# Kernel tuning notes

Hardware: AMD Instinct MI355X
Metric: run time of the kernel (lower is better)

The kernel has to match this reference:

```python
import jax, jax.numpy as jnp
import numpy as np

D_MODEL = 1024
N_HEADS = 16
DH = D_MODEL // N_HEADS
T = 64
NUM_REL = 15 * 15  # (2*7+1)^2 for 8x8 grid
B = 1024


def _build_rel_index(H=8, W=8, dx_max=7, dy_max=7):
    ys, xs = np.meshgrid(np.arange(H), np.arange(W), indexing='ij')
    coords = np.stack([xs.reshape(-1), ys.reshape(-1)], axis=-1)  # [T,2] (x,y)
    disp = coords[None, :, :] - coords[:, None, :]
    dx = np.clip(disp[..., 0], -dx_max, dx_max) + dx_max
    dy = np.clip(disp[..., 1], -dy_max, dy_max) + dy_max
    return jnp.asarray(dx + (2 * dx_max + 1) * dy, dtype=jnp.int32)  # [T,T]


def setup_inputs() -> dict:
    key = jax.random.key(0)
    ks = jax.random.split(key, 12)
    s = 0.02
    return {
        'x': jax.random.normal(ks[0], (B, T, D_MODEL), dtype=jnp.float32),
        'Wq_w': jax.random.normal(ks[1], (D_MODEL, D_MODEL), dtype=jnp.float32) * s,
        'Wq_b': jnp.zeros((D_MODEL,), dtype=jnp.float32),
        'Wk_w': jax.random.normal(ks[2], (D_MODEL, D_MODEL), dtype=jnp.float32) * s,
        'Wk_b': jnp.zeros((D_MODEL,), dtype=jnp.float32),
        'Wv_w': jax.random.normal(ks[3], (D_MODEL, D_MODEL), dtype=jnp.float32) * s,
        'Wv_b': jnp.zeros((D_MODEL,), dtype=jnp.float32),
        'Wo_w': jax.random.normal(ks[4], (D_MODEL, D_MODEL), dtype=jnp.float32) * s,
        'Wo_b': jnp.zeros((D_MODEL,), dtype=jnp.float32),
        'rel_q': jax.random.normal(ks[5], (N_HEADS, NUM_REL, DH), dtype=jnp.float32) * s,
        'rel_k': jax.random.normal(ks[6], (N_HEADS, NUM_REL, DH), dtype=jnp.float32) * s,
        'rel_v': jax.random.normal(ks[7], (N_HEADS, NUM_REL, DH), dtype=jnp.float32) * s,
        'rel_index': _build_rel_index(),
    }


def reference(x, Wq_w, Wq_b, Wk_w, Wk_b, Wv_w, Wv_b, Wo_w, Wo_b,
              rel_q, rel_k, rel_v, rel_index):
    Bb, Tt, D = x.shape
    H, dh = N_HEADS, DH
    scale = 1.0 / jnp.sqrt(jnp.asarray(dh, dtype=x.dtype))
    # projections (torch Linear: x @ W.T + b), split into heads -> [B,H,T,dh]
    q = (x @ Wq_w.T + Wq_b).reshape(Bb, Tt, H, dh).transpose(0, 2, 1, 3)
    k = (x @ Wk_w.T + Wk_b).reshape(Bb, Tt, H, dh).transpose(0, 2, 1, 3)
    v = (x @ Wv_w.T + Wv_b).reshape(Bb, Tt, H, dh).transpose(0, 2, 1, 3)
    # gather relative embeddings -> [H,T,T,dh]
    rq = rel_q[:, rel_index]
    rk = rel_k[:, rel_index]
    rv = rel_v[:, rel_index]
    qk = jnp.einsum('bhtd,bhsd->bhts', q, k)
    q_relk = jnp.einsum('bhtd,htsd->bhts', q, rk)
    relq_k = jnp.einsum('htsd,bhsd->bhts', rq, k)
    relq_relk = jnp.einsum('htsd,htsd->hts', rq, rk)
    logits = (qk + q_relk + relq_k + relq_relk[None]) * scale
    attn = jax.nn.softmax(logits, axis=-1)  # [B,H,T,T]
    out = jnp.einsum('bhts,bhsd->bhtd', attn, v) + jnp.einsum('bhts,htsd->bhtd', attn, rv)
    out = out.transpose(0, 2, 1, 3).reshape(Bb, Tt, D)
    return out @ Wo_w.T + Wo_b
```

## Files before the change

kernel.cpp:

```cpp
#include <hip/hip_runtime.h>

typedef __attribute__((ext_vector_type(4))) float f32x4;
typedef __attribute__((ext_vector_type(8))) short s16x8;
typedef __attribute__((ext_vector_type(4))) short s16x4;

__device__ __forceinline__ short f2bf(float f) {
  union { float f; unsigned u; } v; v.f = f;
  unsigned r = (v.u + 0x7fffu + ((v.u >> 16) & 1u)) >> 16;
  return (short)(r & 0xffffu);
}
__device__ __forceinline__ float bf2f(short s) {
  union { unsigned u; float f; } v; v.u = ((unsigned)(unsigned short)s) << 16;
  return v.f;
}
__device__ __forceinline__ f32x4 mfma16(s16x8 a, s16x8 b, f32x4 c) {
  return __builtin_amdgcn_mfma_f32_16x16x32_bf16(a, b, c, 0, 0, 0);
}

#define AS1(p) ((__attribute__((address_space(1))) void*)(p))
#define AS3(p) ((__attribute__((address_space(3))) void*)(p))

__global__ __launch_bounds__(256) void cvt_bf16_kernel(const float* __restrict__ in,
                                                       short* __restrict__ out, long n) {
  long i = ((long)blockIdx.x * 256 + threadIdx.x) * 4;
  if (i + 4 <= n) {
    f32x4 v = *(const f32x4*)(in + i);
    s16x4 o;
    o[0] = f2bf(v[0]); o[1] = f2bf(v[1]); o[2] = f2bf(v[2]); o[3] = f2bf(v[3]);
    *(s16x4*)(out + i) = o;
  }
}

__global__ __launch_bounds__(256) void bias_cat_kernel(const float* __restrict__ bq,
                                                       const float* __restrict__ bk,
                                                       const float* __restrict__ bv,
                                                       float* __restrict__ o) {
  int i = blockIdx.x * 256 + threadIdx.x;
  if (i < 3072) o[i] = (i < 1024) ? bq[i] : ((i < 2048) ? bk[i - 1024] : bv[i - 2048]);
}

__global__ __launch_bounds__(64) void prep_rel_kernel(
    const float* __restrict__ rq, const float* __restrict__ rk, const float* __restrict__ rv,
    short* __restrict__ relqb, short* __restrict__ relkb, short* __restrict__ relvT,
    float* __restrict__ Dh) {
  int h = blockIdx.x / 240;
  int r = blockIdx.x % 240;
  int d = threadIdx.x;
  float vq = 0.f, vk = 0.f, vv = 0.f;
  if (r < 225) {
    long o = ((long)h * 225 + r) * 64 + d;
    vq = rq[o]; vk = rk[o]; vv = rv[o];
  }
  relqb[((long)h * 240 + r) * 64 + d] = f2bf(vq);
  relkb[((long)h * 240 + r) * 64 + d] = f2bf(vk);
  relvT[((long)h * 64 + d) * 256 + r] = f2bf(vv);
  if (r < 16) relvT[((long)h * 64 + d) * 256 + 240 + r] = 0;
  float p = vq * vk;
  #pragma unroll
  for (int m = 32; m >= 1; m >>= 1) p += __shfl_xor(p, m);
  if (d == 0) Dh[h * 240 + r] = p;
}

#define BAR  __builtin_amdgcn_s_barrier()
#define LGK0 do { asm volatile("s_waitcnt lgkmcnt(0)" ::: "memory"); \
                  __builtin_amdgcn_sched_barrier(0); } while (0)
#define VM0  asm volatile("s_waitcnt vmcnt(0)" ::: "memory")
#define PRIO1 __builtin_amdgcn_s_setprio(1)
#define PRIO0 __builtin_amdgcn_s_setprio(0)

#define STG_A(D, H, KOFF) do { \
    const short* _s = gA + (long)(H) * 128 * ldaL + (KOFF); \
    char* _d = lds + (D) * 32768 + (H) * 16384 + ldsw; \
    __builtin_amdgcn_global_load_lds(AS1(_s), AS3(_d), 16, 0, 0); \
    __builtin_amdgcn_global_load_lds(AS1(_s + 64 * ldaL), AS3(_d + 8192), 16, 0, 0); \
  } while (0)
#define STG_B(D, H, KOFF) do { \
    const short* _s = gB + (long)(H) * 128 * ldbL + (KOFF); \
    char* _d = lds + 65536 + (D) * 32768 + (H) * 16384 + ldsw; \
    __builtin_amdgcn_global_load_lds(AS1(_s), AS3(_d), 16, 0, 0); \
    __builtin_amdgcn_global_load_lds(AS1(_s + 64 * ldbL), AS3(_d + 8192), 16, 0, 0); \
  } while (0)
#define RD_A(D, MIH) do { \
    const char* _b = lds + (D) * 32768 + baseA + (MIH) * 8192; \
    _Pragma("unroll") for (int i = 0; i < 4; i++) { \
      aa[0][i] = *(const s16x8*)(_b + i * 2048 + cax0); \
      aa[1][i] = *(const s16x8*)(_b + i * 2048 + cax1); \
    } } while (0)
#define RD_B(D, NJH) do { \
    const char* _b = lds + (D) * 32768 + baseB + (NJH) * 4096; \
    _Pragma("unroll") for (int j = 0; j < 2; j++) { \
      bb[0][(NJH) * 2 + j] = *(const s16x8*)(_b + j * 2048 + cax0); \
      bb[1][(NJH) * 2 + j] = *(const s16x8*)(_b + j * 2048 + cax1); \
    } } while (0)
#define MM_Q(MIH, NJH) do { \
    _Pragma("unroll") for (int i = 0; i < 4; i++) { \
      _Pragma("unroll") for (int j = 0; j < 2; j++) { \
        f32x4& c = acc[(MIH) * 4 + i][(NJH) * 2 + j]; \
        c = mfma16(bb[0][(NJH) * 2 + j], aa[0][i], c); \
        c = mfma16(bb[1][(NJH) * 2 + j], aa[1][i], c); \
    } } } while (0)

template<int OUT_BF16>
__global__ __launch_bounds__(512, 2) void gemm256_kernel(
    const short* __restrict__ A, const short* __restrict__ Bw,
    const float* __restrict__ bias, void* __restrict__ Cout,
    int N, int K, int lda) {
  __shared__ __attribute__((aligned(16))) char lds[131072];
  const int tid = threadIdx.x, lane = tid & 63, w = tid >> 6;
  const int wr = w >> 2, wc = w & 3;
  const int l15 = lane & 15, l4 = lane >> 4;
  const int nbn = N >> 8;
  const int nwg = gridDim.x, bid = blockIdx.x;
  const int swz = ((bid & 7) * (nwg >> 3)) + (bid >> 3);
  const int bm = swz / nbn, bn = swz % nbn;

  const int srow = tid >> 3;
  const int scol = ((tid & 7) ^ (srow & 7)) * 8;
  const long ldaL = lda, ldbL = K;
  const short* gA = A  + ((long)(bm * 256 + srow)) * ldaL + scol;
  const short* gB = Bw + ((long)(bn * 256 + srow)) * ldbL + scol;
  const int ldsw = w * 1024;

  const int baseA = (wr * 128 + l15) * 128;
  const int baseB = 65536 + (wc * 64 + l15) * 128;
  const int cax0 = ((l4) ^ (l15 & 7)) * 16;
  const int cax1 = ((4 + l4) ^ (l15 & 7)) * 16;

  f32x4 acc[8][4];
  #pragma unroll
  for (int i = 0; i < 8; i++)
    #pragma unroll
    for (int j = 0; j < 4; j++) acc[i][j] = (f32x4){0.f, 0.f, 0.f, 0.f};
  s16x8 aa[2][4], bb[2][4];

  STG_A(0, 0, 0); STG_A(0, 1, 0); STG_B(0, 0, 0); STG_B(0, 1, 0);
  STG_B(1, 0, 64); STG_B(1, 1, 64);
  VM0;
  BAR;

  const int NT = K >> 6;
  for (int kt = 0; kt < NT; kt += 2) {
    const int k1 = (kt + 1) << 6, k2 = (kt + 2) << 6, k3 = (kt + 3) << 6;
    const bool full = (kt + 2) < NT;
    STG_A(1, 0, k1);
    RD_A(0, 0); RD_B(0, 0);
    BAR; LGK0; PRIO1; MM_Q(0, 0); PRIO0; BAR;
    STG_A(1, 1, k1);
    RD_B(0, 1);
    BAR; LGK0; PRIO1; MM_Q(0, 1); PRIO0; BAR;
    if (full) STG_B(0, 0, k2);
    RD_A(0, 1);
    BAR; LGK0; PRIO1; MM_Q(1, 0); PRIO0; BAR;
    if (full) STG_B(0, 1, k2);
    BAR; LGK0; PRIO1; MM_Q(1, 1); PRIO0;
    VM0;
    BAR;
    if (full) STG_A(0, 0, k2);
    RD_A(1, 0); RD_B(1, 0);
    BAR; LGK0; PRIO1; MM_Q(0, 0); PRIO0; BAR;
    if (full) STG_A(0, 1, k2);
    RD_B(1, 1);
    BAR; LGK0; PRIO1; MM_Q(0, 1); PRIO0; BAR;
    if (full) STG_B(1, 0, k3);
    RD_A(1, 1);
    BAR; LGK0; PRIO1; MM_Q(1, 0); PRIO0; BAR;
    if (full) STG_B(1, 1, k3);
    BAR; LGK0; PRIO1; MM_Q(1, 1); PRIO0;
    VM0;
    BAR;
  }

  const long crow = (long)bm * 256 + wr * 128;
  const int ccol = bn * 256 + wc * 64;
  #pragma unroll
  for (int nj = 0; nj < 4; nj++) {
    const int colb = ccol + nj * 16 + l4 * 4;
    const f32x4 bv4 = *(const f32x4*)&bias[colb];
    #pragma unroll
    for (int mi = 0; mi < 8; mi++) {
      const long row = crow + mi * 16 + l15;
      f32x4 v = acc[mi][nj] + bv4;
      if (OUT_BF16) {
        s16x4 o;
        o[0] = f2bf(v[0]); o[1] = f2bf(v[1]); o[2] = f2bf(v[2]); o[3] = f2bf(v[3]);
        *(s16x4*)((short*)Cout + row * N + colb) = o;
      } else {
        *(f32x4*)((float*)Cout + row * N + colb) = v;
      }
    }
  }
}

__global__ __launch_bounds__(256, 2) void attn_kernel(
    const short* __restrict__ qkv, const short* __restrict__ relqb,
    const short* __restrict__ relkb, const float* __restrict__ Dh,
    const short* __restrict__ relvT, const int* __restrict__ rel_index,
    short* __restrict__ aout) {
  __shared__ __attribute__((aligned(16))) char region[65536];
  __shared__ __attribute__((aligned(16))) char vts[8192];

  const int tid = threadIdx.x, lane = tid & 63, w = tid >> 6;
  const int l15 = lane & 15, l4 = lane >> 4;
  const int bh = blockIdx.x, b = bh >> 4, h = bh & 15;
  const f32x4 zero = {0.f, 0.f, 0.f, 0.f};

  {
    const int t = tid >> 2, c0 = (tid & 3) * 16;
    const long g = ((long)(b * 64 + t)) * 3072 + 2048 + h * 64 + c0;
    s16x8 v0 = *(const s16x8*)(qkv + g);
    s16x8 v1 = *(const s16x8*)(qkv + g + 8);
    #pragma unroll
    for (int i = 0; i < 8; i++) {
      const int d = c0 + i;
      *(short*)(vts + d * 128 + ((t * 2) ^ ((d & 7) << 4))) = v0[i];
    }
    #pragma unroll
    for (int i = 0; i < 8; i++) {
      const int d = c0 + 8 + i;
      *(short*)(vts + d * 128 + ((t * 2) ^ ((d & 7) << 4))) = v1[i];
    }
  }

  const long qbase = ((long)(b * 64 + w * 16 + l15)) * 3072 + h * 64;
  s16x8 aq0 = *(const s16x8*)(qkv + qbase + l4 * 8);
  s16x8 aq1 = *(const s16x8*)(qkv + qbase + 32 + l4 * 8);
  s16x8 ak0 = *(const s16x8*)(qkv + qbase + 1024 + l4 * 8);
  s16x8 ak1 = *(const s16x8*)(qkv + qbase + 1056 + l4 * 8);

  f32x4 sacc[4];
  sacc[0] = sacc[1] = sacc[2] = sacc[3] = zero;
  #pragma unroll
  for (int n = 0; n < 4; n++) {
    const long kb = ((long)(b * 64 + n * 16 + l15)) * 3072 + 1024 + h * 64;
    s16x8 b0 = *(const s16x8*)(qkv + kb + l4 * 8);
    s16x8 b1 = *(const s16x8*)(qkv + kb + 32 + l4 * 8);
    sacc[n] = mfma16(aq0, b0, sacc[n]);
    sacc[n] = mfma16(aq1, b1, sacc[n]);
  }

  char* qw  = region + w * 8192;
  char* krs = region + 32768;
  const short* rkh = relkb + (long)h * 240 * 64;
  const short* rqh = relqb + (long)h * 240 * 64;
  const int rowk = w * 16 + l15;
  #pragma unroll
  for (int nj = 0; nj < 15; nj++) {
    const int rr = nj * 16 + l15;
    s16x8 b0 = *(const s16x8*)(rkh + rr * 64 + l4 * 8);
    s16x8 b1 = *(const s16x8*)(rkh + rr * 64 + 32 + l4 * 8);
    f32x4 t0 = mfma16(b1, aq1, mfma16(b0, aq0, zero));
    s16x8 c0v = *(const s16x8*)(rqh + rr * 64 + l4 * 8);
    s16x8 c1v = *(const s16x8*)(rqh + rr * 64 + 32 + l4 * 8);
    f32x4 t1 = mfma16(c1v, ak1, mfma16(c0v, ak0, zero));
    const f32x4 dv4 = *(const f32x4*)&Dh[h * 240 + nj * 16 + l4 * 4];
    const int cb = (nj * 32 + l4 * 8) ^ ((l15 & 7) << 4);
    s16x4 q4, k4;
    #pragma unroll
    for (int j = 0; j < 4; j++) { q4[j] = f2bf(t0[j] + dv4[j]); k4[j] = f2bf(t1[j]); }
    *(s16x4*)(qw + l15 * 512 + cb) = q4;
    *(s16x4*)(krs + rowk * 512 + cb) = k4;
  }
  __syncthreads();

  #pragma unroll
  for (int n = 0; n < 4; n++)
    #pragma unroll
    for (int j = 0; j < 4; j++) {
      const int tl = l4 * 4 + j;
      const int t = w * 16 + tl, s = n * 16 + l15;
      const int r = rel_index[t * 64 + s];
      const float qg = bf2f(*(const short*)(qw + tl * 512 + ((r * 2) ^ ((tl & 7) << 4))));
      const float kg = bf2f(*(const short*)(krs + s * 512 + ((r * 2) ^ ((s & 7) << 4))));
      sacc[n][j] = (sacc[n][j] + qg + kg) * 0.125f;
    }
  float att[4][4];
  #pragma unroll
  for (int j = 0; j < 4; j++) {
    float m = fmaxf(fmaxf(sacc[0][j], sacc[1][j]), fmaxf(sacc[2][j], sacc[3][j]));
    m = fmaxf(m, __shfl_xor(m, 1));
    m = fmaxf(m, __shfl_xor(m, 2));
    m = fmaxf(m, __shfl_xor(m, 4));
    m = fmaxf(m, __shfl_xor(m, 8));
    float sum = 0.f;
    #pragma unroll
    for (int n = 0; n < 4; n++) { att[n][j] = __expf(sacc[n][j] - m); sum += att[n][j]; }
    sum += __shfl_xor(sum, 1);
    sum += __shfl_xor(sum, 2);
    sum += __shfl_xor(sum, 4);
    sum += __shfl_xor(sum, 8);
    const float inv = 1.f / sum;
    #pragma unroll
    for (int n = 0; n < 4; n++) att[n][j] *= inv;
  }
  __syncthreads();

  char* Pb = region;
  {
    s16x8 z = {0, 0, 0, 0, 0, 0, 0, 0};
    #pragma unroll
    for (int i = 0; i < 8; i++) {
      const int c = lane + 64 * i;
      *(s16x8*)(Pb + (w * 16 + (c >> 5)) * 640 + (c & 31) * 16) = z;
    }
  }
  #pragma unroll
  for (int n = 0; n < 4; n++)
    #pragma unroll
    for (int j = 0; j < 4; j++) {
      const int t = w * 16 + l4 * 4 + j, s = n * 16 + l15;
      const int r = rel_index[t * 64 + s];
      const int sw = (t & 7) << 4;
      const short a = f2bf(att[n][j]);
      *(short*)(Pb + t * 640 + ((r * 2) ^ sw)) = a;
      *(short*)(Pb + t * 640 + 512 + ((s * 2) ^ sw)) = a;
    }

  f32x4 oacc[4];
  oacc[0] = oacc[1] = oacc[2] = oacc[3] = zero;
  const int rowp = w * 16 + l15, px = (rowp & 7) << 4;
  const short* rvh = relvT + (long)h * 16384;
  #pragma unroll
  for (int kk = 0; kk < 8; kk++) {
    s16x8 pa = *(const s16x8*)(Pb + rowp * 640 + ((kk * 64 + l4 * 16) ^ px));
    #pragma unroll
    for (int m = 0; m < 4; m++) {
      s16x8 bbv = *(const s16x8*)(rvh + (m * 16 + l15) * 256 + kk * 32 + l4 * 8);
      oacc[m] = mfma16(bbv, pa, oacc[m]);
    }
  }
  #pragma unroll
  for (int ks = 0; ks < 2; ks++) {
    s16x8 pa = *(const s16x8*)(Pb + rowp * 640 + 512 + ((ks * 64 + l4 * 16) ^ px));
    #pragma unroll
    for (int m = 0; m < 4; m++) {
      const int d = m * 16 + l15;
      s16x8 bbv = *(const s16x8*)(vts + d * 128 + ((ks * 64 + l4 * 16) ^ ((d & 7) << 4)));
      oacc[m] = mfma16(bbv, pa, oacc[m]);
    }
  }
  const long obase = ((long)(b * 64 + w * 16 + l15)) * 1024 + h * 64;
  #pragma unroll
  for (int m = 0; m < 4; m++) {
    s16x4 o;
    o[0] = f2bf(oacc[m][0]); o[1] = f2bf(oacc[m][1]);
    o[2] = f2bf(oacc[m][2]); o[3] = f2bf(oacc[m][3]);
    *(s16x4*)(aout + obase + m * 16 + l4 * 4) = o;
  }
}

extern "C" void kernel_launch(void* const* d_in, const int* in_sizes, int n_in,
                              void* d_out, int out_size, void* d_ws, size_t ws_size,
                              hipStream_t stream) {
  const float* x     = (const float*)d_in[0];
  const float* Wq_w  = (const float*)d_in[1];
  const float* Wq_b  = (const float*)d_in[2];
  const float* Wk_w  = (const float*)d_in[3];
  const float* Wk_b  = (const float*)d_in[4];
  const float* Wv_w  = (const float*)d_in[5];
  const float* Wv_b  = (const float*)d_in[6];
  const float* Wo_w  = (const float*)d_in[7];
  const float* Wo_b  = (const float*)d_in[8];
  const float* rel_q = (const float*)d_in[9];
  const float* rel_k = (const float*)d_in[10];
  const float* rel_v = (const float*)d_in[11];
  const int* rel_index = (const int*)d_in[12];
  float* out = (float*)d_out;

  char* ws = (char*)d_ws;
  short* x_bf   = (short*)(ws);
  short* qkv_bf = (short*)(ws + 134217728L);
  short* wq_bf  = (short*)(ws + 536870912L);
  short* wo_bf  = (short*)(ws + 543162368L);
  float* biascat= (float*)(ws + 545259520L);
  short* relqb  = (short*)(ws + 545271808L);
  short* relkb  = (short*)(ws + 545763328L);
  short* relvT  = (short*)(ws + 546254848L);
  float* Dh     = (float*)(ws + 546779136L);
  short* aout   = x_bf;

  cvt_bf16_kernel<<<65536, 256, 0, stream>>>(x, x_bf, 67108864L);
  cvt_bf16_kernel<<<1024, 256, 0, stream>>>(Wq_w, wq_bf, 1048576L);
  cvt_bf16_kernel<<<1024, 256, 0, stream>>>(Wk_w, (short*)(ws + 538968064L), 1048576L);
  cvt_bf16_kernel<<<1024, 256, 0, stream>>>(Wv_w, (short*)(ws + 541065216L), 1048576L);
  cvt_bf16_kernel<<<1024, 256, 0, stream>>>(Wo_w, wo_bf, 1048576L);
  bias_cat_kernel<<<12, 256, 0, stream>>>(Wq_b, Wk_b, Wv_b, biascat);
  prep_rel_kernel<<<3840, 64, 0, stream>>>(rel_q, rel_k, rel_v, relqb, relkb, relvT, Dh);

  gemm256_kernel<1><<<3072, 512, 0, stream>>>(x_bf, wq_bf, biascat, (void*)qkv_bf,
                                              3072, 1024, 1024);
  attn_kernel<<<16384, 256, 0, stream>>>(qkv_bf, relqb, relkb, Dh, relvT, rel_index, aout);
  gemm256_kernel<0><<<1024, 512, 0, stream>>>(aout, wo_bf, Wo_b, (void*)out,
                                              1024, 1024, 1024);
}
```

Measured before the change: 1.567 ms.

## Split attention block into Q-side and K/V-side wave groups with 512 threads

Doubles the attention block to 512 threads. Waves 0-3 handle the Q·K scores and the Q·relK table, while waves 4-7 do the V transpose and the relQ·K table concurrently. The P·V stage is then split so each of the eight waves computes two of the four output column tiles. The relative-index lookups are also preloaded into registers, which removes repeated global loads. The aim is to shorten the per-block critical path and raise the number of waves available to hide latency, at the cost of an extra barrier and more threads sitting idle in the softmax phase.

Result: faster. 1.493 ms (-4.8%).

```diff
diff --git a/kernel.cpp b/kernel.cpp
--- a/kernel.cpp
+++ b/kernel.cpp
@@ -191,7 +191,7 @@
   }
 }
 
-__global__ __launch_bounds__(256, 2) void attn_kernel(
+__global__ __launch_bounds__(512, 4) void attn_kernel(
     const short* __restrict__ qkv, const short* __restrict__ relqb,
     const short* __restrict__ relkb, const float* __restrict__ Dh,
     const short* __restrict__ relvT, const int* __restrict__ rel_index,
@@ -204,147 +204,167 @@
   const int bh = blockIdx.x, b = bh >> 4, h = bh & 15;
   const f32x4 zero = {0.f, 0.f, 0.f, 0.f};
 
-  {
-    const int t = tid >> 2, c0 = (tid & 3) * 16;
-    const long g = ((long)(b * 64 + t)) * 3072 + 2048 + h * 64 + c0;
+  char* qw  = region + (w & 3) * 8192;
+  char* krs = region + 32768;
+
+  f32x4 sacc[4];
+  float att[4][4];
+  int idxr[16];
+  s16x8 aq0, aq1;
+
+  if (w < 4) {
+    #pragma unroll
+    for (int n = 0; n < 4; n++)
+      #pragma unroll
+      for (int j = 0; j < 4; j++)
+        idxr[n * 4 + j] = rel_index[(w * 16 + l4 * 4 + j) * 64 + n * 16 + l15];
+    const long qb = ((long)(b * 64 + w * 16 + l15)) * 3072 + h * 64;
+    aq0 = *(const s16x8*)(qkv + qb + l4 * 8);
+    aq1 = *(const s16x8*)(qkv + qb + 32 + l4 * 8);
+    sacc[0] = sacc[1] = sacc[2] = sacc[3] = zero;
+    #pragma unroll
+    for (int n = 0; n < 4; n++) {
+      const long kb = ((long)(b * 64 + n * 16 + l15)) * 3072 + 1024 + h * 64;
+      s16x8 b0 = *(const s16x8*)(qkv + kb + l4 * 8);
+      s16x8 b1 = *(const s16x8*)(qkv + kb + 32 + l4 * 8);
+      sacc[n] = mfma16(aq0, b0, sacc[n]);
+      sacc[n] = mfma16(aq1, b1, sacc[n]);
+    }
+    const short* rkh = relkb + (long)h * 240 * 64;
+    #pragma unroll
+    for (int nj = 0; nj < 15; nj++) {
+      const int rr = nj * 16 + l15;
+      s16x8 b0 = *(const s16x8*)(rkh + rr * 64 + l4 * 8);
+      s16x8 b1 = *(const s16x8*)(rkh + rr * 64 + 32 + l4 * 8);
+      f32x4 t0 = mfma16(b1, aq1, mfma16(b0, aq0, zero));
+      const f32x4 dv4 = *(const f32x4*)&Dh[h * 240 + nj * 16 + l4 * 4];
+      const int cb = (nj * 32 + l4 * 8) ^ ((l15 & 7) << 4);
+      s16x4 q4;
+      #pragma unroll
+      for (int j = 0; j < 4; j++) q4[j] = f2bf(t0[j] + dv4[j]);
+      *(s16x4*)(qw + l15 * 512 + cb) = q4;
+    }
+  } else {
+    const int tid2 = tid - 256;
+    const int tv = tid2 >> 2, c0 = (tid2 & 3) * 16;
+    const long g = ((long)(b * 64 + tv)) * 3072 + 2048 + h * 64 + c0;
     s16x8 v0 = *(const s16x8*)(qkv + g);
     s16x8 v1 = *(const s16x8*)(qkv + g + 8);
     #pragma unroll
     for (int i = 0; i < 8; i++) {
       const int d = c0 + i;
-      *(short*)(vts + d * 128 + ((t * 2) ^ ((d & 7) << 4))) = v0[i];
+      *(short*)(vts + d * 128 + ((tv * 2) ^ ((d & 7) << 4))) = v0[i];
     }
     #pragma unroll
     for (int i = 0; i < 8; i++) {
       const int d = c0 + 8 + i;
-      *(short*)(vts + d * 128 + ((t * 2) ^ ((d & 7) << 4))) = v1[i];
-    }
-  }
-
-  const long qbase = ((long)(b * 64 + w * 16 + l15)) * 3072 + h * 64;
-  s16x8 aq0 = *(const s16x8*)(qkv + qbase + l4 * 8);
-  s16x8 aq1 = *(const s16x8*)(qkv + qbase + 32 + l4 * 8);
-  s16x8 ak0 = *(const s16x8*)(qkv + qbase + 1024 + l4 * 8);
-  s16x8 ak1 = *(const s16x8*)(qkv + qbase + 1056 + l4 * 8);
-
-  f32x4 sacc[4];
-  sacc[0] = sacc[1] = sacc[2] = sacc[3] = zero;
-  #pragma unroll
-  for (int n = 0; n < 4; n++) {
-    const long kb = ((long)(b * 64 + n * 16 + l15)) * 3072 + 1024 + h * 64;
-    s16x8 b0 = *(const s16x8*)(qkv + kb + l4 * 8);
-    s16x8 b1 = *(const s16x8*)(qkv + kb + 32 + l4 * 8);
-    sacc[n] = mfma16(aq0, b0, sacc[n]);
-    sacc[n] = mfma16(aq1, b1, sacc[n]);
-  }
-
-  char* qw  = region + w * 8192;
-  char* krs = region + 32768;
-  const short* rkh = relkb + (long)h * 240 * 64;
-  const short* rqh = relqb + (long)h * 240 * 64;
-  const int rowk = w * 16 + l15;
-  #pragma unroll
-  for (int nj = 0; nj < 15; nj++) {
-    const int rr = nj * 16 + l15;
-    s16x8 b0 = *(const s16x8*)(rkh + rr * 64 + l4 * 8);
-    s16x8 b1 = *(const s16x8*)(rkh + rr * 64 + 32 + l4 * 8);
-    f32x4 t0 = mfma16(b1, aq1, mfma16(b0, aq0, zero));
-    s16x8 c0v = *(const s16x8*)(rqh + rr * 64 + l4 * 8);
-    s16x8 c1v = *(const s16x8*)(rqh + rr * 64 + 32 + l4 * 8);
-    f32x4 t1 = mfma16(c1v, ak1, mfma16(c0v, ak0, zero));
-    const f32x4 dv4 = *(const f32x4*)&Dh[h * 240 + nj * 16 + l4 * 4];
-    const int cb = (nj * 32 + l4 * 8) ^ ((l15 & 7) << 4);
-    s16x4 q4, k4;
-    #pragma unroll
-    for (int j = 0; j < 4; j++) { q4[j] = f2bf(t0[j] + dv4[j]); k4[j] = f2bf(t1[j]); }
-    *(s16x4*)(qw + l15 * 512 + cb) = q4;
-    *(s16x4*)(krs + rowk * 512 + cb) = k4;
+      *(short*)(vts + d * 128 + ((tv * 2) ^ ((d & 7) << 4))) = v1[i];
+    }
+    const int wl = w - 4;
+    const int rowk = wl * 16 + l15;
+    const long kb2 = ((long)(b * 64 + rowk)) * 3072 + 1024 + h * 64;
+    s16x8 ak0 = *(const s16x8*)(qkv + kb2 + l4 * 8);
+    s16x8 ak1 = *(const s16x8*)(qkv + kb2 + 32 + l4 * 8);
+    const short* rqh = relqb + (long)h * 240 * 64;
+    #pragma unroll
+    for (int nj = 0; nj < 15; nj++) {
+      const int rr = nj * 16 + l15;
+      s16x8 c0v = *(const s16x8*)(rqh + rr * 64 + l4 * 8);
+      s16x8 c1v = *(const s16x8*)(rqh + rr * 64 + 32 + l4 * 8);
+      f32x4 t1 = mfma16(c1v, ak1, mfma16(c0v, ak0, zero));
+      const int cb = (nj * 32 + l4 * 8) ^ ((l15 & 7) << 4);
+      s16x4 k4;
+      #pragma unroll
+      for (int j = 0; j < 4; j++) k4[j] = f2bf(t1[j]);
+      *(s16x4*)(krs + rowk * 512 + cb) = k4;
+    }
   }
   __syncthreads();
 
-  #pragma unroll
-  for (int n = 0; n < 4; n++)
+  if (w < 4) {
+    #pragma unroll
+    for (int n = 0; n < 4; n++)
+      #pragma unroll
+      for (int j = 0; j < 4; j++) {
+        const int tl = l4 * 4 + j;
+        const int s = n * 16 + l15;
+        const int r = idxr[n * 4 + j];
+        const float qg = bf2f(*(const short*)(qw + tl * 512 + ((r * 2) ^ ((tl & 7) << 4))));
+        const float kg = bf2f(*(const short*)(krs + s * 512 + ((r * 2) ^ ((s & 7) << 4))));
+        sacc[n][j] = (sacc[n][j] + qg + kg) * 0.125f;
+      }
     #pragma unroll
     for (int j = 0; j < 4; j++) {
-      const int tl = l4 * 4 + j;
-      const int t = w * 16 + tl, s = n * 16 + l15;
-      const int r = rel_index[t * 64 + s];
-      const float qg = bf2f(*(const short*)(qw + tl * 512 + ((r * 2) ^ ((tl & 7) << 4))));
-      const float kg = bf2f(*(const short*)(krs + s * 512 + ((r * 2) ^ ((s & 7) << 4))));
-      sacc[n][j] = (sacc[n][j] + qg + kg) * 0.125f;
-    }
-  float att[4][4];
-  #pragma unroll
-  for (int j = 0; j < 4; j++) {
-    float m = fmaxf(fmaxf(sacc[0][j], sacc[1][j]), fmaxf(sacc[2][j], sacc[3][j]));
-    m = fmaxf(m, __shfl_xor(m, 1));
-    m = fmaxf(m, __shfl_xor(m, 2));
-    m = fmaxf(m, __shfl_xor(m, 4));
-    m = fmaxf(m, __shfl_xor(m, 8));
-    float sum = 0.f;
-    #pragma unroll
-    for (int n = 0; n < 4; n++) { att[n][j] = __expf(sacc[n][j] - m); sum += att[n][j]; }
-    sum += __shfl_xor(sum, 1);
-    sum += __shfl_xor(sum, 2);
-    sum += __shfl_xor(sum, 4);
-    sum += __shfl_xor(sum, 8);
-    const float inv = 1.f / sum;
-    #pragma unroll
-    for (int n = 0; n < 4; n++) att[n][j] *= inv;
+      float m = fmaxf(fmaxf(sacc[0][j], sacc[1][j]), fmaxf(sacc[2][j], sacc[3][j]));
+      m = fmaxf(m, __shfl_xor(m, 1));
+      m = fmaxf(m, __shfl_xor(m, 2));
+      m = fmaxf(m, __shfl_xor(m, 4));
+      m = fmaxf(m, __shfl_xor(m, 8));
+      float sum = 0.f;
+      #pragma unroll
+      for (int n = 0; n < 4; n++) { att[n][j] = __expf(sacc[n][j] - m); sum += att[n][j]; }
+      sum += __shfl_xor(sum, 1);
+      sum += __shfl_xor(sum, 2);
+      sum += __shfl_xor(sum, 4);
+      sum += __shfl_xor(sum, 8);
+      const float inv = 1.f / sum;
+      #pragma unroll
+      for (int n = 0; n < 4; n++) att[n][j] *= inv;
+    }
   }
   __syncthreads();
 
   char* Pb = region;
-  {
+  if (w < 4) {
     s16x8 z = {0, 0, 0, 0, 0, 0, 0, 0};
     #pragma unroll
     for (int i = 0; i < 8; i++) {
       const int c = lane + 64 * i;
       *(s16x8*)(Pb + (w * 16 + (c >> 5)) * 640 + (c & 31) * 16) = z;
     }
-  }
-  #pragma unroll
-  for (int n = 0; n < 4; n++)
-    #pragma unroll
-    for (int j = 0; j < 4; j++) {
-      const int t = w * 16 + l4 * 4 + j, s = n * 16 + l15;
-      const int r = rel_index[t * 64 + s];
-      const int sw = (t & 7) << 4;
-      const short a = f2bf(att[n][j]);
-      *(short*)(Pb + t * 640 + ((r * 2) ^ sw)) = a;
-      *(short*)(Pb + t * 640 + 512 + ((s * 2) ^ sw)) = a;
-    }
-
-  f32x4 oacc[4];
-  oacc[0] = oacc[1] = oacc[2] = oacc[3] = zero;
-  const int rowp = w * 16 + l15, px = (rowp & 7) << 4;
+    #pragma unroll
+    for (int n = 0; n < 4; n++)
+      #pragma unroll
+      for (int j = 0; j < 4; j++) {
+        const int t = w * 16 + l4 * 4 + j, s = n * 16 + l15;
+        const int r = idxr[n * 4 + j];
+        const int sw = (t & 7) << 4;
+        const short a = f2bf(att[n][j]);
+        *(short*)(Pb + t * 640 + ((r * 2) ^ sw)) = a;
+        *(short*)(Pb + t * 640 + 512 + ((s * 2) ^ sw)) = a;
+      }
+  }
+  __syncthreads();
+
+  const int tc = w & 3, mb = (w >> 2) * 2;
+  const int rowp = tc * 16 + l15, px = (rowp & 7) << 4;
   const short* rvh = relvT + (long)h * 16384;
+  f32x4 oacc0 = zero, oacc1 = zero;
   #pragma unroll
   for (int kk = 0; kk < 8; kk++) {
     s16x8 pa = *(const s16x8*)(Pb + rowp * 640 + ((kk * 64 + l4 * 16) ^ px));
-    #pragma unroll
-    for (int m = 0; m < 4; m++) {
-      s16x8 bbv = *(const s16x8*)(rvh + (m * 16 + l15) * 256 + kk * 32 + l4 * 8);
-      oacc[m] = mfma16(bbv, pa, oacc[m]);
-    }
+    s16x8 bv0 = *(const s16x8*)(rvh + ((mb + 0) * 16 + l15) * 256 + kk * 32 + l4 * 8);
+    s16x8 bv1 = *(const s16x8*)(rvh + ((mb + 1) * 16 + l15) * 256 + kk * 32 + l4 * 8);
+    oacc0 = mfma16(bv0, pa, oacc0);
+    oacc1 = mfma16(bv1, pa, oacc1);
   }
   #pragma unroll
   for (int ks = 0; ks < 2; ks++) {
     s16x8 pa = *(const s16x8*)(Pb + rowp * 640 + 512 + ((ks * 64 + l4 * 16) ^ px));
-    #pragma unroll
-    for (int m = 0; m < 4; m++) {
-      const int d = m * 16 + l15;
-      s16x8 bbv = *(const s16x8*)(vts + d * 128 + ((ks * 64 + l4 * 16) ^ ((d & 7) << 4)));
-      oacc[m] = mfma16(bbv, pa, oacc[m]);
-    }
-  }
-  const long obase = ((long)(b * 64 + w * 16 + l15)) * 1024 + h * 64;
-  #pragma unroll
-  for (int m = 0; m < 4; m++) {
-    s16x4 o;
-    o[0] = f2bf(oacc[m][0]); o[1] = f2bf(oacc[m][1]);
-    o[2] = f2bf(oacc[m][2]); o[3] = f2bf(oacc[m][3]);
-    *(s16x4*)(aout + obase + m * 16 + l4 * 4) = o;
+    const int d0 = (mb + 0) * 16 + l15;
+    const int d1 = (mb + 1) * 16 + l15;
+    s16x8 bv0 = *(const s16x8*)(vts + d0 * 128 + ((ks * 64 + l4 * 16) ^ ((d0 & 7) << 4)));
+    s16x8 bv1 = *(const s16x8*)(vts + d1 * 128 + ((ks * 64 + l4 * 16) ^ ((d1 & 7) << 4)));
+    oacc0 = mfma16(bv0, pa, oacc0);
+    oacc1 = mfma16(bv1, pa, oacc1);
+  }
+  const long obase = ((long)(b * 64 + rowp)) * 1024 + h * 64 + l4 * 4;
+  {
+    s16x4 o0, o1;
+    #pragma unroll
+    for (int j = 0; j < 4; j++) { o0[j] = f2bf(oacc0[j]); o1[j] = f2bf(oacc1[j]); }
+    *(s16x4*)(aout + obase + (mb + 0) * 16) = o0;
+    *(s16x4*)(aout + obase + (mb + 1) * 16) = o1;
   }
 }
 
@@ -388,7 +408,7 @@
 
   gemm256_kernel<1><<<3072, 512, 0, stream>>>(x_bf, wq_bf, biascat, (void*)qkv_bf,
                                               3072, 1024, 1024);
-  attn_kernel<<<16384, 256, 0, stream>>>(qkv_bf, relqb, relkb, Dh, relvT, rel_index, aout);
+  attn_kernel<<<16384, 512, 0, stream>>>(qkv_bf, relqb, relkb, Dh, relvT, rel_index, aout);
   gemm256_kernel<0><<<1024, 512, 0, stream>>>(aout, wo_bf, Wo_b, (void*)out,
                                               1024, 1024, 1024);
 }
```
